# Performance work log

Measured on AMD Instinct MI355X. Metric: run time of the kernel, lower is better.

## Reference

```python
import jax, jax.numpy as jnp
import numpy as np

N_TOTAL = 2_000_000
B = 50_000
D_MODEL = 128
HIDDEN = 64


def setup_inputs() -> dict:
    key = jax.random.key(0)
    ks = jax.random.split(key, 5)
    h = jax.random.normal(ks[0], (N_TOTAL, D_MODEL), dtype=jnp.float32)
    segment_ids = jnp.sort(jax.random.randint(ks[1], (N_TOTAL,), 0, B, dtype=jnp.int32))
    # MLP params (Linear stores [out,in] in torch; we use [in,out] with x @ W)
    W1 = jax.random.normal(ks[2], (D_MODEL, HIDDEN), dtype=jnp.float32) * (1.0 / np.sqrt(D_MODEL))
    b1 = jnp.zeros((HIDDEN,), dtype=jnp.float32)
    W2 = jax.random.normal(ks[3], (HIDDEN, HIDDEN), dtype=jnp.float32) * (1.0 / np.sqrt(HIDDEN))
    b2 = jnp.zeros((HIDDEN,), dtype=jnp.float32)
    W3 = jax.random.normal(ks[4], (HIDDEN, 1), dtype=jnp.float32) * (1.0 / np.sqrt(HIDDEN))
    b3 = jnp.zeros((1,), dtype=jnp.float32)
    return {"h": h, "segment_ids": segment_ids, "num_segments": B,
            "W1": W1, "b1": b1, "W2": W2, "b2": b2, "W3": W3, "b3": b3}


def reference(h, segment_ids, num_segments, W1, b1, W2, b2, W3, b3):
    # Ragged mean pooling over atoms -> [B, d_model] (fused segment reduce)
    sums = jax.ops.segment_sum(h, segment_ids, num_segments=num_segments)
    counts = jax.ops.segment_sum(jnp.ones((h.shape[0],), h.dtype), segment_ids,
                                 num_segments=num_segments)
    pooled = sums / jnp.maximum(counts, 1.0)[:, None]  # [B, d_model]
    # 3-layer MLP with SiLU -> scalar per molecule
    x = jax.nn.silu(pooled @ W1 + b1)
    x = jax.nn.silu(x @ W2 + b2)
    scalar = (x @ W3 + b3)[:, 0]  # [B]
    return scalar
```

## Files before the change

### kernel.cpp

```cpp
#include <hip/hip_runtime.h>

#define D_MODEL 128
#define HIDDEN 64
#define WPB 8
#define NTHREADS (WPB * 64)
#define NBLOCKS 512
#define W1_STRIDE 132
#define W2_STRIDE 68
#define SEG_BATCH 4

__global__ void seg_bounds_kernel(const int* __restrict__ seg, int n, int B,
                                  int* __restrict__ seg_start) {
  int i = blockIdx.x * blockDim.x + threadIdx.x;
  if (i >= n) return;
  int s = seg[i];
  if (i == 0) {
    for (int t = 0; t <= s; ++t) seg_start[t] = 0;
  } else {
    int p = seg[i - 1];
    for (int t = p + 1; t <= s; ++t) seg_start[t] = i;
  }
  if (i == n - 1) {
    for (int t = s + 1; t <= B; ++t) seg_start[t] = n;
  }
}

__device__ __forceinline__ float silu(float x) {
  return x / (1.0f + __expf(-x));
}
__device__ __forceinline__ float4 f4add(float4 a, float4 b) {
  return make_float4(a.x + b.x, a.y + b.y, a.z + b.z, a.w + b.w);
}
__device__ __forceinline__ float wave_sum(float p) {
#pragma unroll
  for (int off = 32; off >= 1; off >>= 1) p += __shfl_xor(p, off);
  return p;
}

__global__ __launch_bounds__(NTHREADS, 4) void pool_mlp_kernel(
    const float* __restrict__ h, const int* __restrict__ seg_start,
    const float* __restrict__ W1, const float* __restrict__ b1,
    const float* __restrict__ W2, const float* __restrict__ b2,
    const float* __restrict__ W3, const float* __restrict__ b3,
    float* __restrict__ out, int B, int n_atoms) {
  __shared__ float sW1T[HIDDEN * W1_STRIDE];
  __shared__ float sW2T[HIDDEN * W2_STRIDE];
  __shared__ float pooled_lds[WPB][SEG_BATCH][D_MODEL];
  __shared__ float x1_lds[WPB][SEG_BATCH][HIDDEN];

  const int tid = threadIdx.x;

#pragma unroll
  for (int i = tid; i < (D_MODEL * HIDDEN) / 4; i += NTHREADS) {
    float4 v = reinterpret_cast<const float4*>(W1)[i];
    int k = i >> 4;
    int j = (4 * i) & (HIDDEN - 1);
    sW1T[(j + 0) * W1_STRIDE + k] = v.x;
    sW1T[(j + 1) * W1_STRIDE + k] = v.y;
    sW1T[(j + 2) * W1_STRIDE + k] = v.z;
    sW1T[(j + 3) * W1_STRIDE + k] = v.w;
  }
#pragma unroll
  for (int i = tid; i < (HIDDEN * HIDDEN) / 4; i += NTHREADS) {
    float4 v = reinterpret_cast<const float4*>(W2)[i];
    int k = i >> 4;
    int j = (4 * i) & (HIDDEN - 1);
    sW2T[(j + 0) * W2_STRIDE + k] = v.x;
    sW2T[(j + 1) * W2_STRIDE + k] = v.y;
    sW2T[(j + 2) * W2_STRIDE + k] = v.z;
    sW2T[(j + 3) * W2_STRIDE + k] = v.w;
  }
  __syncthreads();

  const int wave = tid >> 6;
  const int lane = tid & 63;
  const float b1l = b1[lane];
  const float b2l = b2[lane];
  const float w3l = W3[lane];
  const float b3l = b3[0];

  const int G = gridDim.x * WPB;
  const int g = blockIdx.x * WPB + wave;
  const int base = B / G;
  const int rem = B - base * G;
  const int my_cnt = base + (g < rem ? 1 : 0);
  const int my_s0 = g * base + (g < rem ? g : rem);
  if (my_cnt == 0) return;

  const int half = lane >> 5;
  const int l32 = lane & 31;
  const float4* __restrict__ hv = reinterpret_cast<const float4*>(h);
  const float4* __restrict__ w1v =
      reinterpret_cast<const float4*>(&sW1T[lane * W1_STRIDE]);
  const float4* __restrict__ w2v =
      reinterpret_cast<const float4*>(&sW2T[lane * W2_STRIDE]);

  float4 pf0, pf1, pf2, pf3;
  bool have_pf = false;

  int start = seg_start[my_s0];
  for (int si = 0; si < my_cnt; si += SEG_BATCH) {
    const int nb = min(SEG_BATCH, my_cnt - si);

    for (int b = 0; b < nb; ++b) {
      const int end = seg_start[my_s0 + si + b + 1];
      const int cnt = end - start;
      float4 acc0 = make_float4(0.f, 0.f, 0.f, 0.f);
      float4 acc1 = acc0, acc2 = acc0, acc3 = acc0;
      int a = start + half;
      if (have_pf) {
        if (a < end) acc0 = f4add(acc0, pf0);
        if (a + 2 < end) acc1 = f4add(acc1, pf1);
        if (a + 4 < end) acc2 = f4add(acc2, pf2);
        if (a + 6 < end) acc3 = f4add(acc3, pf3);
        a += 8;
        have_pf = false;
      }
      for (; a + 6 < end; a += 8) {
        float4 v0 = hv[(a + 0) * 32 + l32];
        float4 v1 = hv[(a + 2) * 32 + l32];
        float4 v2 = hv[(a + 4) * 32 + l32];
        float4 v3 = hv[(a + 6) * 32 + l32];
        acc0 = f4add(acc0, v0);
        acc1 = f4add(acc1, v1);
        acc2 = f4add(acc2, v2);
        acc3 = f4add(acc3, v3);
      }
      if (a < end) {
        const int c1 = min(a + 2, n_atoms - 1);
        const int c2 = min(a + 4, n_atoms - 1);
        float4 v0 = hv[a * 32 + l32];
        float4 v1 = hv[c1 * 32 + l32];
        float4 v2 = hv[c2 * 32 + l32];
        acc0 = f4add(acc0, v0);
        if (a + 2 < end) acc1 = f4add(acc1, v1);
        if (a + 4 < end) acc2 = f4add(acc2, v2);
      }
      acc0 = f4add(f4add(acc0, acc1), f4add(acc2, acc3));
      acc0.x += __shfl_xor(acc0.x, 32);
      acc0.y += __shfl_xor(acc0.y, 32);
      acc0.z += __shfl_xor(acc0.z, 32);
      acc0.w += __shfl_xor(acc0.w, 32);
      const float inv = 1.0f / (float)max(cnt, 1);
      if (half == 0) {
        reinterpret_cast<float4*>(&pooled_lds[wave][b][0])[l32] = make_float4(
            acc0.x * inv, acc0.y * inv, acc0.z * inv, acc0.w * inv);
      }
      start = end;
    }
    __builtin_amdgcn_wave_barrier();

    if (si + SEG_BATCH < my_cnt) {
      const int pa = start + half;
      const int c0 = min(pa + 0, n_atoms - 1);
      const int c1 = min(pa + 2, n_atoms - 1);
      const int c2 = min(pa + 4, n_atoms - 1);
      const int c3 = min(pa + 6, n_atoms - 1);
      pf0 = hv[c0 * 32 + l32];
      pf1 = hv[c1 * 32 + l32];
      pf2 = hv[c2 * 32 + l32];
      pf3 = hv[c3 * 32 + l32];
      have_pf = true;
    }

    const float4* pv0 = reinterpret_cast<const float4*>(&pooled_lds[wave][0][0]);
    const float4* pv1 = reinterpret_cast<const float4*>(&pooled_lds[wave][1][0]);
    const float4* pv2 = reinterpret_cast<const float4*>(&pooled_lds[wave][2][0]);
    const float4* pv3 = reinterpret_cast<const float4*>(&pooled_lds[wave][3][0]);
    float a1b0 = b1l, a1b1 = b1l, a1b2 = b1l, a1b3 = b1l;
#pragma unroll 8
    for (int t = 0; t < D_MODEL / 4; ++t) {
      float4 w = w1v[t];
      float4 p0 = pv0[t], p1 = pv1[t], p2 = pv2[t], p3 = pv3[t];
      a1b0 = fmaf(p0.x, w.x, a1b0); a1b0 = fmaf(p0.y, w.y, a1b0);
      a1b0 = fmaf(p0.z, w.z, a1b0); a1b0 = fmaf(p0.w, w.w, a1b0);
      a1b1 = fmaf(p1.x, w.x, a1b1); a1b1 = fmaf(p1.y, w.y, a1b1);
      a1b1 = fmaf(p1.z, w.z, a1b1); a1b1 = fmaf(p1.w, w.w, a1b1);
      a1b2 = fmaf(p2.x, w.x, a1b2); a1b2 = fmaf(p2.y, w.y, a1b2);
      a1b2 = fmaf(p2.z, w.z, a1b2); a1b2 = fmaf(p2.w, w.w, a1b2);
      a1b3 = fmaf(p3.x, w.x, a1b3); a1b3 = fmaf(p3.y, w.y, a1b3);
      a1b3 = fmaf(p3.z, w.z, a1b3); a1b3 = fmaf(p3.w, w.w, a1b3);
    }
    x1_lds[wave][0][lane] = silu(a1b0);
    x1_lds[wave][1][lane] = silu(a1b1);
    x1_lds[wave][2][lane] = silu(a1b2);
    x1_lds[wave][3][lane] = silu(a1b3);
    __builtin_amdgcn_wave_barrier();

    const float4* x10 = reinterpret_cast<const float4*>(&x1_lds[wave][0][0]);
    const float4* x11 = reinterpret_cast<const float4*>(&x1_lds[wave][1][0]);
    const float4* x12 = reinterpret_cast<const float4*>(&x1_lds[wave][2][0]);
    const float4* x13 = reinterpret_cast<const float4*>(&x1_lds[wave][3][0]);
    float a2b0 = b2l, a2b1 = b2l, a2b2 = b2l, a2b3 = b2l;
#pragma unroll 8
    for (int t = 0; t < HIDDEN / 4; ++t) {
      float4 w = w2v[t];
      float4 p0 = x10[t], p1 = x11[t], p2 = x12[t], p3 = x13[t];
      a2b0 = fmaf(p0.x, w.x, a2b0); a2b0 = fmaf(p0.y, w.y, a2b0);
      a2b0 = fmaf(p0.z, w.z, a2b0); a2b0 = fmaf(p0.w, w.w, a2b0);
      a2b1 = fmaf(p1.x, w.x, a2b1); a2b1 = fmaf(p1.y, w.y, a2b1);
      a2b1 = fmaf(p1.z, w.z, a2b1); a2b1 = fmaf(p1.w, w.w, a2b1);
      a2b2 = fmaf(p2.x, w.x, a2b2); a2b2 = fmaf(p2.y, w.y, a2b2);
      a2b2 = fmaf(p2.z, w.z, a2b2); a2b2 = fmaf(p2.w, w.w, a2b2);
      a2b3 = fmaf(p3.x, w.x, a2b3); a2b3 = fmaf(p3.y, w.y, a2b3);
      a2b3 = fmaf(p3.z, w.z, a2b3); a2b3 = fmaf(p3.w, w.w, a2b3);
    }
    float r0 = wave_sum(silu(a2b0) * w3l);
    float r1 = wave_sum(silu(a2b1) * w3l);
    float r2 = wave_sum(silu(a2b2) * w3l);
    float r3 = wave_sum(silu(a2b3) * w3l);
    float val = (lane == 0) ? r0 : (lane == 1) ? r1 : (lane == 2) ? r2 : r3;
    if (lane < nb) out[my_s0 + si + lane] = val + b3l;
  }
}

extern "C" void kernel_launch(void* const* d_in, const int* in_sizes, int n_in,
                              void* d_out, int out_size, void* d_ws, size_t ws_size,
                              hipStream_t stream) {
  const float* h = (const float*)d_in[0];
  const int* seg = (const int*)d_in[1];
  const float* W1 = (const float*)d_in[3];
  const float* b1 = (const float*)d_in[4];
  const float* W2 = (const float*)d_in[5];
  const float* b2 = (const float*)d_in[6];
  const float* W3 = (const float*)d_in[7];
  const float* b3 = (const float*)d_in[8];
  float* out = (float*)d_out;

  const int n = in_sizes[1];
  const int B = out_size;

  int* seg_start = (int*)d_ws;

  {
    int threads = 256;
    int blocks = (n + threads - 1) / threads;
    seg_bounds_kernel<<<blocks, threads, 0, stream>>>(seg, n, B, seg_start);
  }
  {
    pool_mlp_kernel<<<NBLOCKS, NTHREADS, 0, stream>>>(
        h, seg_start, W1, b1, W2, b2, W3, b3, out, B, n);
  }
}
```

Measured before the change: 199.0 us.

## Balance waves by atom count, deepen load unroll, drop cross-batch prefetch

Work is now split across waves by equal atom ranges, using a binary search over segment starts, rather than by equal segment counts. This balances the memory traffic each wave handles. The atom loop unrolls to 16 rows per iteration with an 8-row tail, and each batch's segment ends are loaded up front. The prefetch of the next batch across the MLP phase is removed, and the binary searches overlap the weight staging before the barrier, at the cost of some per-wave setup latency.

```diff
diff --git a/kernel.cpp b/kernel.cpp
--- a/kernel.cpp
+++ b/kernel.cpp
@@ -36,6 +36,15 @@
   for (int off = 32; off >= 1; off >>= 1) p += __shfl_xor(p, off);
   return p;
 }
+__device__ __forceinline__ int lower_bound_ge(const int* __restrict__ arr,
+                                              int B, int target) {
+  int lo = 0, hi = B;
+  while (lo < hi) {
+    int m = (lo + hi) >> 1;
+    if (arr[m] >= target) hi = m; else lo = m + 1;
+  }
+  return lo;
+}
 
 __global__ __launch_bounds__(NTHREADS, 4) void pool_mlp_kernel(
     const float* __restrict__ h, const int* __restrict__ seg_start,
@@ -70,22 +79,25 @@
     sW2T[(j + 2) * W2_STRIDE + k] = v.z;
     sW2T[(j + 3) * W2_STRIDE + k] = v.w;
   }
-  __syncthreads();
 
   const int wave = tid >> 6;
   const int lane = tid & 63;
+
+  const int G = gridDim.x * WPB;
+  const int g = blockIdx.x * WPB + wave;
+  const int lo = (int)(((long long)g * n_atoms) / G);
+  const int hi = (int)(((long long)(g + 1) * n_atoms) / G);
+  const int my_s0 = lower_bound_ge(seg_start, B, lo);
+  int s_end = (g == G - 1) ? B : lower_bound_ge(seg_start, B, hi);
+  const int my_cnt = s_end - my_s0;
+
+  __syncthreads();
+  if (my_cnt <= 0) return;
+
   const float b1l = b1[lane];
   const float b2l = b2[lane];
   const float w3l = W3[lane];
   const float b3l = b3[0];
-
-  const int G = gridDim.x * WPB;
-  const int g = blockIdx.x * WPB + wave;
-  const int base = B / G;
-  const int rem = B - base * G;
-  const int my_cnt = base + (g < rem ? 1 : 0);
-  const int my_s0 = g * base + (g < rem ? g : rem);
-  if (my_cnt == 0) return;
 
   const int half = lane >> 5;
   const int l32 = lane & 31;
@@ -95,36 +107,44 @@
   const float4* __restrict__ w2v =
       reinterpret_cast<const float4*>(&sW2T[lane * W2_STRIDE]);
 
-  float4 pf0, pf1, pf2, pf3;
-  bool have_pf = false;
-
   int start = seg_start[my_s0];
   for (int si = 0; si < my_cnt; si += SEG_BATCH) {
     const int nb = min(SEG_BATCH, my_cnt - si);
 
+    int ends[SEG_BATCH];
+#pragma unroll
+    for (int b = 0; b < SEG_BATCH; ++b) {
+      ends[b] = seg_start[my_s0 + si + min(b, nb - 1) + 1];
+    }
+
     for (int b = 0; b < nb; ++b) {
-      const int end = seg_start[my_s0 + si + b + 1];
+      const int end = ends[b];
       const int cnt = end - start;
       float4 acc0 = make_float4(0.f, 0.f, 0.f, 0.f);
       float4 acc1 = acc0, acc2 = acc0, acc3 = acc0;
       int a = start + half;
-      if (have_pf) {
-        if (a < end) acc0 = f4add(acc0, pf0);
-        if (a + 2 < end) acc1 = f4add(acc1, pf1);
-        if (a + 4 < end) acc2 = f4add(acc2, pf2);
-        if (a + 6 < end) acc3 = f4add(acc3, pf3);
-        a += 8;
-        have_pf = false;
-      }
-      for (; a + 6 < end; a += 8) {
+      for (; a + 14 < end; a += 16) {
         float4 v0 = hv[(a + 0) * 32 + l32];
         float4 v1 = hv[(a + 2) * 32 + l32];
         float4 v2 = hv[(a + 4) * 32 + l32];
         float4 v3 = hv[(a + 6) * 32 + l32];
-        acc0 = f4add(acc0, v0);
-        acc1 = f4add(acc1, v1);
-        acc2 = f4add(acc2, v2);
-        acc3 = f4add(acc3, v3);
+        float4 v4 = hv[(a + 8) * 32 + l32];
+        float4 v5 = hv[(a + 10) * 32 + l32];
+        float4 v6 = hv[(a + 12) * 32 + l32];
+        float4 v7 = hv[(a + 14) * 32 + l32];
+        acc0 = f4add(acc0, v0); acc1 = f4add(acc1, v1);
+        acc2 = f4add(acc2, v2); acc3 = f4add(acc3, v3);
+        acc0 = f4add(acc0, v4); acc1 = f4add(acc1, v5);
+        acc2 = f4add(acc2, v6); acc3 = f4add(acc3, v7);
+      }
+      if (a + 6 < end) {
+        float4 v0 = hv[(a + 0) * 32 + l32];
+        float4 v1 = hv[(a + 2) * 32 + l32];
+        float4 v2 = hv[(a + 4) * 32 + l32];
+        float4 v3 = hv[(a + 6) * 32 + l32];
+        acc0 = f4add(acc0, v0); acc1 = f4add(acc1, v1);
+        acc2 = f4add(acc2, v2); acc3 = f4add(acc3, v3);
+        a += 8;
       }
       if (a < end) {
         const int c1 = min(a + 2, n_atoms - 1);
@@ -149,19 +169,6 @@
       start = end;
     }
     __builtin_amdgcn_wave_barrier();
-
-    if (si + SEG_BATCH < my_cnt) {
-      const int pa = start + half;
-      const int c0 = min(pa + 0, n_atoms - 1);
-      const int c1 = min(pa + 2, n_atoms - 1);
-      const int c2 = min(pa + 4, n_atoms - 1);
-      const int c3 = min(pa + 6, n_atoms - 1);
-      pf0 = hv[c0 * 32 + l32];
-      pf1 = hv[c1 * 32 + l32];
-      pf2 = hv[c2 * 32 + l32];
-      pf3 = hv[c3 * 32 + l32];
-      have_pf = true;
-    }
 
     const float4* pv0 = reinterpret_cast<const float4*>(&pooled_lds[wave][0][0]);
     const float4* pv1 = reinterpret_cast<const float4*>(&pooled_lds[wave][1][0]);
```

After: 206.4 us. 3.7% more time.
